# Kernel optimization log

Hardware: AMD Instinct MI355X
Metric: run time of the kernel (lower is better)

Reference implementation:

```python
import jax, jax.numpy as jnp
import numpy as np
from jax.scipy.special import logsumexp

TEMPERATURE = 0.1
EPS = 1e-8  # matches torch F.cosine_similarity eps


def setup_inputs() -> dict:
    key = jax.random.key(0)
    k1, k2 = jax.random.split(key)
    N, D, NUM_CLASSES = 8192, 256, 64
    embeddings = jax.random.normal(k1, (N, D), dtype=jnp.float32)
    target = jax.random.randint(k2, (N,), 0, NUM_CLASSES, dtype=jnp.int64)
    return {"embeddings": embeddings, "target": target}


def reference(embeddings, target):
    N = target.shape[0]
    # cosine similarity: normalize rows, then a single GEMM for all pairs
    norms = jnp.linalg.norm(embeddings, axis=-1, keepdims=True)
    e = embeddings / jnp.maximum(norms, EPS)
    sim = (e @ e.T) / TEMPERATURE  # [N, N]

    pos = target[:, None] == target[None, :]  # [N, N] bool, incl. diagonal
    diag = jnp.eye(N, dtype=bool)
    neg_inf = jnp.asarray(-jnp.inf, dtype=sim.dtype)

    # denominator: negatives only (positives masked to -inf)
    lse_neg = logsumexp(jnp.where(pos, neg_inf, sim), axis=1)
    # numerator: positives excluding self (diagonal masked to -inf)
    lse_pos = logsumexp(jnp.where(pos & ~diag, sim, neg_inf), axis=1)

    loss = lse_neg - lse_pos
    return loss.sum()
```

## Files before the change

kernel.cpp:

```cpp
#include <hip/hip_runtime.h>
#include <hip/hip_bf16.h>
#include <stdint.h>
#include <math.h>

#define NROWS 8192
#define DIM   256
#define RB    256
#define BI    128
#define JSUB  64
#define NBJS  8
#define JBLK  (JSUB*NBJS)
#define NG    (NROWS/JBLK)
#define NIT   (NROWS/BI)
#define NCLS  64
#define CAP   256

typedef __attribute__((ext_vector_type(4)))  int   int4v;
typedef __attribute__((ext_vector_type(8)))  int   int8v;
typedef __attribute__((ext_vector_type(16))) float floatx16;

typedef const __attribute__((address_space(1))) uint32_t gas_u32;
typedef __attribute__((address_space(3))) uint32_t las_u32;

#define SCALE_1_16 0x7B7B7B7B
#define L2E10      14.4269504088896f
#define CA_SCALE   (L2E10 * 16.0f)
#define CB_SCALE   16.0f

#if __has_builtin(__builtin_amdgcn_exp2f)
#define EXP2(x) __builtin_amdgcn_exp2f(x)
#else
#define EXP2(x) exp2f(x)
#endif

__device__ __forceinline__ void gload_lds16(const void* g, void* l) {
    __builtin_amdgcn_global_load_lds((gas_u32*)(uintptr_t)g,
                                     (las_u32*)(uintptr_t)l, 16, 0, 0);
}

__global__ __launch_bounds__(256) void normalize_kernel(const float* __restrict__ emb,
                                                        uint32_t* __restrict__ a8,
                                                        uint32_t* __restrict__ b8,
                                                        float* __restrict__ out)
{
    if (blockIdx.x == 0 && threadIdx.x == 0) *out = 0.f;
    int row  = blockIdx.x * 4 + (threadIdx.x >> 6);
    int lane = threadIdx.x & 63;
    float4 v = ((const float4*)(emb + (size_t)row * DIM))[lane];
    float ss = v.x*v.x + v.y*v.y + v.z*v.z + v.w*v.w;
    #pragma unroll
    for (int off = 32; off > 0; off >>= 1)
        ss += __shfl_xor(ss, off, 64);
    float inv = 1.0f / fmaxf(sqrtf(ss), 1e-8f);
    float ia = CA_SCALE * inv, ib = CB_SCALE * inv;
    int ra = __builtin_amdgcn_cvt_pk_fp8_f32(v.x * ia, v.y * ia, 0, false);
    ra     = __builtin_amdgcn_cvt_pk_fp8_f32(v.z * ia, v.w * ia, ra, true);
    int rb = __builtin_amdgcn_cvt_pk_fp8_f32(v.x * ib, v.y * ib, 0, false);
    rb     = __builtin_amdgcn_cvt_pk_fp8_f32(v.z * ib, v.w * ib, rb, true);
    a8[(size_t)row * 64 + lane] = (uint32_t)ra;
    b8[(size_t)row * 64 + lane] = (uint32_t)rb;
}

template<bool DIAG>
__device__ __forceinline__ void epi(const floatx16 acc[2],
                                    int jbs, int h, int ic0, float& ts)
{
    #pragma unroll
    for (int jt = 0; jt < 2; ++jt)
        #pragma unroll
        for (int rq = 0; rq < 4; ++rq)
            #pragma unroll
            for (int r2 = 0; r2 < 4; ++r2) {
                float v = EXP2(acc[jt][rq * 4 + r2]);
                if (DIAG) {
                    const int jg_ = jbs + jt * 32 + rq * 8 + h * 4 + r2;
                    if (jg_ == ic0) v = 0.f;
                }
                ts += v;
            }
}

__global__ __launch_bounds__(256, 4) void fused_kernel(const uint8_t* __restrict__ eA,
                                                       const uint8_t* __restrict__ eB,
                                                       const int* __restrict__ tgt,
                                                       float* __restrict__ pts,
                                                       float* __restrict__ sp)
{
    __shared__ uint8_t smem[2 * JSUB * RB];

    const int bi   = blockIdx.x;
    const int jg   = blockIdx.y;
    const int tid  = threadIdx.x;
    const int wave = tid >> 6;
    const int lane = tid & 63;
    const int col  = lane & 31;
    const int h    = lane >> 5;

    const uint8_t* pbB = eB + (size_t)(bi * BI + wave * 32 + col) * RB + h * 32;
    int8v bfr[4];
    #pragma unroll
    for (int s = 0; s < 4; ++s)
        bfr[s] = *(const int8v*)(pbB + s * 64);

    int goffA[4];
    #pragma unroll
    for (int t = 0; t < 4; ++t) {
        int s   = wave * 256 + t * 64 + lane;
        int row = s >> 4;
        int lc  = (s & 15) ^ (row & 15);
        goffA[t] = row * RB + lc * 16;
    }
    const char* gA = (const char*)(eA + (size_t)jg * JBLK * RB);

    #pragma unroll
    for (int t = 0; t < 4; ++t)
        gload_lds16(gA + goffA[t], smem + wave * 4096 + t * 1024);

    const int ic0 = bi * BI + wave * 32 + col;

    const int xm = col & 15;
    int poff[4];
    #pragma unroll
    for (int s = 0; s < 4; ++s)
        poff[s] = ((s * 4 + h * 2) ^ xm) << 4;

    __syncthreads();

    float ts = 0.f;
    const int dpair = bi - jg * 4;

    #pragma unroll
    for (int bjs = 0; bjs < NBJS; ++bjs) {
        if (bjs < NBJS - 1) {
            const char* gAn = gA + (size_t)(bjs + 1) * JSUB * RB;
            #pragma unroll
            for (int t = 0; t < 4; ++t)
                gload_lds16(gAn + goffA[t],
                            smem + ((bjs + 1) & 1) * (JSUB * RB) + wave * 4096 + t * 1024);
        }

        const uint8_t* ab = smem + (bjs & 1) * (JSUB * RB);
        floatx16 acc[2];
        #pragma unroll
        for (int jt = 0; jt < 2; ++jt)
            acc[jt] = (floatx16){0.f,0.f,0.f,0.f,0.f,0.f,0.f,0.f,
                                 0.f,0.f,0.f,0.f,0.f,0.f,0.f,0.f};

        #pragma unroll
        for (int s = 0; s < 4; ++s) {
            int8v af[2];
            #pragma unroll
            for (int jt = 0; jt < 2; ++jt) {
                const uint8_t* pa = ab + (size_t)(jt * 32 + col) * RB;
                int4v lo = *(const int4v*)(pa + poff[s]);
                int4v hi = *(const int4v*)(pa + (poff[s] ^ 16));
                af[jt] = __builtin_shufflevector(lo, hi, 0, 1, 2, 3, 4, 5, 6, 7);
            }
            #pragma unroll
            for (int jt = 0; jt < 2; ++jt)
                acc[jt] = __builtin_amdgcn_mfma_scale_f32_32x32x64_f8f6f4(
                    af[jt], bfr[s], acc[jt], 0, 0,
                    0, SCALE_1_16, 0, SCALE_1_16);
        }

        const int jbs = jg * JBLK + bjs * JSUB;
        if ((bjs >> 1) == dpair)
            epi<true >(acc, jbs, h, ic0, ts);
        else
            epi<false>(acc, jbs, h, ic0, ts);

        if (bjs < NBJS - 1)
            __syncthreads();
    }

    ts += __shfl_xor(ts, 32, 64);
    if (h == 0)
        pts[(size_t)jg * NROWS + ic0] = ts;

    if (jg != (bi >> 2)) return;
    const int c = bi;

    __syncthreads();
    int* idx = (int*)smem;
    int* cnt = (int*)(smem + CAP * 4);
    if (tid == 0) *cnt = 0;
    __syncthreads();
    int4v tv[8];
    #pragma unroll
    for (int k = 0; k < 8; ++k)
        tv[k] = *(const int4v*)(tgt + k * 1024 + tid * 4);
    #pragma unroll
    for (int k = 0; k < 8; ++k)
        #pragma unroll
        for (int r = 0; r < 4; ++r)
            if (tv[k][r] == c) {
                int p = atomicAdd(cnt, 1);
                if (p < CAP) idx[p] = k * 1024 + tid * 4 + r;
            }
    __syncthreads();
    const int M   = min(*cnt, CAP);
    const int Mp  = (M + 31) & ~31;
    const int nbt = Mp >> 5;

    for (int bt = wave; bt < nbt; bt += 4) {
        const int b = bt * 32 + col;
        const uint8_t* pb = eB + (size_t)idx[min(b, M - 1)] * RB + h * 32;
        int8v bpr[4];
        #pragma unroll
        for (int s = 0; s < 4; ++s)
            bpr[s] = *(const int8v*)(pb + s * 64);
        float psum = 0.f;
        for (int at = 0; at < nbt; ++at) {
            const uint8_t* pa = eA + (size_t)idx[min(at * 32 + col, M - 1)] * RB + h * 32;
            floatx16 acc = (floatx16){0.f,0.f,0.f,0.f,0.f,0.f,0.f,0.f,
                                      0.f,0.f,0.f,0.f,0.f,0.f,0.f,0.f};
            #pragma unroll
            for (int s = 0; s < 4; ++s) {
                int8v af = *(const int8v*)(pa + s * 64);
                acc = __builtin_amdgcn_mfma_scale_f32_32x32x64_f8f6f4(
                    af, bpr[s], acc, 0, 0, 0, SCALE_1_16, 0, SCALE_1_16);
            }
            #pragma unroll
            for (int rq = 0; rq < 4; ++rq)
                #pragma unroll
                for (int r2 = 0; r2 < 4; ++r2) {
                    const int a = at * 32 + rq * 8 + h * 4 + r2;
                    float v = EXP2(acc[rq * 4 + r2]);
                    psum += (a != b && a < M) ? v : 0.f;
                }
        }
        psum += __shfl_xor(psum, 32, 64);
        if (h == 0 && b < M) sp[idx[b]] = psum;
    }
}

__global__ __launch_bounds__(256) void finalize_kernel(const float* __restrict__ pts,
                                                       const float* __restrict__ sp,
                                                       float* __restrict__ out)
{
    const int i = blockIdx.x * 256 + threadIdx.x;
    float st = 0.f;
    #pragma unroll
    for (int t = 0; t < NG; ++t)
        st += pts[(size_t)t * NROWS + i];
    const float spv = sp[i];
    const float ns  = st - spv;
    float loss = logf(ns) - logf(spv);
    #pragma unroll
    for (int off = 32; off > 0; off >>= 1)
        loss += __shfl_xor(loss, off, 64);
    __shared__ float w4[4];
    if ((threadIdx.x & 63) == 0) w4[threadIdx.x >> 6] = loss;
    __syncthreads();
    if (threadIdx.x == 0)
        atomicAdd(out, w4[0] + w4[1] + w4[2] + w4[3]);
}

extern "C" void kernel_launch(void* const* d_in, const int* in_sizes, int n_in,
                              void* d_out, int out_size, void* d_ws, size_t ws_size,
                              hipStream_t stream)
{
    (void)in_sizes; (void)n_in; (void)out_size; (void)ws_size;
    const float* emb = (const float*)d_in[0];
    const int*   tgt = (const int*)d_in[1];
    float*       out = (float*)d_out;

    uint32_t* a8  = (uint32_t*)d_ws;
    uint32_t* b8  = a8 + (size_t)NROWS * 64;
    float*    pts = (float*)(b8 + (size_t)NROWS * 64);
    float*    sp  = pts + (size_t)NG * NROWS;

    normalize_kernel<<<NROWS / 4, 256, 0, stream>>>(emb, a8, b8, out);

    dim3 grid(NIT, NG);
    fused_kernel<<<grid, 256, 0, stream>>>(
        (const uint8_t*)a8, (const uint8_t*)b8, tgt, pts, sp);

    finalize_kernel<<<NROWS / 256, 256, 0, stream>>>(pts, sp, out);
}
```

Baseline: 97.47 us.

## Hoist class bucketing into a separate kernel and spread positive-pair tiles across blocks

Moves the per-class index bucketing out of the fused kernel into a small bucket_kernel that also zeroes the positive-sum buffer. The same-class positive-sum work, previously done serially by one block per class (one block in each of 16 groups of the grid), is now split so that each wave across the class's 16 blocks computes one 32x32 tile and accumulates into sp with atomicAdd. This removes the tail where a few blocks did extra serial MFMA loops, at the cost of an extra kernel launch and float atomics, which are nondeterministic.

After: 89.50 us. 8.2% less time.

```diff
diff --git a/kernel.cpp b/kernel.cpp
--- a/kernel.cpp
+++ b/kernel.cpp
@@ -61,6 +61,30 @@
     b8[(size_t)row * 64 + lane] = (uint32_t)rb;
 }
 
+__global__ __launch_bounds__(256) void bucket_kernel(const int* __restrict__ tgt,
+                                                     int* __restrict__ cidx,
+                                                     int* __restrict__ ccnt,
+                                                     float* __restrict__ sp)
+{
+    __shared__ int cnt;
+    const int c = blockIdx.x, tid = threadIdx.x;
+    if (tid == 0) cnt = 0;
+    if (tid < 128) sp[c * 128 + tid] = 0.f;
+    __syncthreads();
+    #pragma unroll
+    for (int k = 0; k < 8; ++k) {
+        int4v tv = *(const int4v*)(tgt + k * 1024 + tid * 4);
+        #pragma unroll
+        for (int r = 0; r < 4; ++r)
+            if (tv[r] == c) {
+                int p = atomicAdd(&cnt, 1);
+                if (p < CAP) cidx[c * CAP + p] = k * 1024 + tid * 4 + r;
+            }
+    }
+    __syncthreads();
+    if (tid == 0) ccnt[c] = min(cnt, CAP);
+}
+
 template<bool DIAG>
 __device__ __forceinline__ void epi(const floatx16 acc[2],
                                     int jbs, int h, int ic0, float& ts)
@@ -82,7 +106,8 @@
 
 __global__ __launch_bounds__(256, 4) void fused_kernel(const uint8_t* __restrict__ eA,
                                                        const uint8_t* __restrict__ eB,
-                                                       const int* __restrict__ tgt,
+                                                       const int* __restrict__ cidx,
+                                                       const int* __restrict__ ccnt,
                                                        float* __restrict__ pts,
                                                        float* __restrict__ sp)
 {
@@ -177,61 +202,46 @@
     if (h == 0)
         pts[(size_t)jg * NROWS + ic0] = ts;
 
-    if (jg != (bi >> 2)) return;
-    const int c = bi;
-
-    __syncthreads();
-    int* idx = (int*)smem;
-    int* cnt = (int*)(smem + CAP * 4);
-    if (tid == 0) *cnt = 0;
-    __syncthreads();
-    int4v tv[8];
-    #pragma unroll
-    for (int k = 0; k < 8; ++k)
-        tv[k] = *(const int4v*)(tgt + k * 1024 + tid * 4);
-    #pragma unroll
-    for (int k = 0; k < 8; ++k)
-        #pragma unroll
-        for (int r = 0; r < 4; ++r)
-            if (tv[k][r] == c) {
-                int p = atomicAdd(cnt, 1);
-                if (p < CAP) idx[p] = k * 1024 + tid * 4 + r;
-            }
-    __syncthreads();
-    const int M   = min(*cnt, CAP);
-    const int Mp  = (M + 31) & ~31;
-    const int nbt = Mp >> 5;
-
-    for (int bt = wave; bt < nbt; bt += 4) {
-        const int b = bt * 32 + col;
-        const uint8_t* pb = eB + (size_t)idx[min(b, M - 1)] * RB + h * 32;
-        int8v bpr[4];
-        #pragma unroll
-        for (int s = 0; s < 4; ++s)
-            bpr[s] = *(const int8v*)(pb + s * 64);
-        float psum = 0.f;
-        for (int at = 0; at < nbt; ++at) {
-            const uint8_t* pa = eA + (size_t)idx[min(at * 32 + col, M - 1)] * RB + h * 32;
-            floatx16 acc = (floatx16){0.f,0.f,0.f,0.f,0.f,0.f,0.f,0.f,
-                                      0.f,0.f,0.f,0.f,0.f,0.f,0.f,0.f};
-            #pragma unroll
-            for (int s = 0; s < 4; ++s) {
-                int8v af = *(const int8v*)(pa + s * 64);
-                acc = __builtin_amdgcn_mfma_scale_f32_32x32x64_f8f6f4(
-                    af, bpr[s], acc, 0, 0, 0, SCALE_1_16, 0, SCALE_1_16);
-            }
-            #pragma unroll
-            for (int rq = 0; rq < 4; ++rq)
-                #pragma unroll
-                for (int r2 = 0; r2 < 4; ++r2) {
-                    const int a = at * 32 + rq * 8 + h * 4 + r2;
-                    float v = EXP2(acc[rq * 4 + r2]);
-                    psum += (a != b && a < M) ? v : 0.f;
-                }
+    const int c   = bi;
+    const int M   = ccnt[c];
+    const int nbt = (M + 31) >> 5;
+    const int w64 = jg * 4 + wave;
+    const int bt  = w64 >> 3;
+    const int at  = w64 & 7;
+    if (bt >= nbt || at >= nbt) return;
+
+    const int* idx = cidx + c * CAP;
+    const int b    = bt * 32 + col;
+    const int bidx = idx[min(b, M - 1)];
+
+    const uint8_t* pb2 = eB + (size_t)bidx * RB + h * 32;
+    int8v bpr[4];
+    #pragma unroll
+    for (int s = 0; s < 4; ++s)
+        bpr[s] = *(const int8v*)(pb2 + s * 64);
+
+    const uint8_t* pa2 = eA + (size_t)idx[min(at * 32 + col, M - 1)] * RB + h * 32;
+    floatx16 acc2 = (floatx16){0.f,0.f,0.f,0.f,0.f,0.f,0.f,0.f,
+                               0.f,0.f,0.f,0.f,0.f,0.f,0.f,0.f};
+    #pragma unroll
+    for (int s = 0; s < 4; ++s) {
+        int8v af = *(const int8v*)(pa2 + s * 64);
+        acc2 = __builtin_amdgcn_mfma_scale_f32_32x32x64_f8f6f4(
+            af, bpr[s], acc2, 0, 0, 0, SCALE_1_16, 0, SCALE_1_16);
+    }
+
+    float psum = 0.f;
+    #pragma unroll
+    for (int rq = 0; rq < 4; ++rq)
+        #pragma unroll
+        for (int r2 = 0; r2 < 4; ++r2) {
+            const int a = at * 32 + rq * 8 + h * 4 + r2;
+            float v = EXP2(acc2[rq * 4 + r2]);
+            psum += (a != b && a < M) ? v : 0.f;
         }
-        psum += __shfl_xor(psum, 32, 64);
-        if (h == 0 && b < M) sp[idx[b]] = psum;
-    }
+    psum += __shfl_xor(psum, 32, 64);
+    if (h == 0 && b < M)
+        atomicAdd(&sp[bidx], psum);
 }
 
 __global__ __launch_bounds__(256) void finalize_kernel(const float* __restrict__ pts,
@@ -265,16 +275,20 @@
     const int*   tgt = (const int*)d_in[1];
     float*       out = (float*)d_out;
 
-    uint32_t* a8  = (uint32_t*)d_ws;
-    uint32_t* b8  = a8 + (size_t)NROWS * 64;
-    float*    pts = (float*)(b8 + (size_t)NROWS * 64);
-    float*    sp  = pts + (size_t)NG * NROWS;
+    uint32_t* a8   = (uint32_t*)d_ws;
+    uint32_t* b8   = a8 + (size_t)NROWS * 64;
+    float*    pts  = (float*)(b8 + (size_t)NROWS * 64);
+    float*    sp   = pts + (size_t)NG * NROWS;
+    int*      cidx = (int*)(sp + NROWS);
+    int*      ccnt = cidx + NCLS * CAP;
 
     normalize_kernel<<<NROWS / 4, 256, 0, stream>>>(emb, a8, b8, out);
+
+    bucket_kernel<<<NCLS, 256, 0, stream>>>(tgt, cidx, ccnt, sp);
 
     dim3 grid(NIT, NG);
     fused_kernel<<<grid, 256, 0, stream>>>(
-        (const uint8_t*)a8, (const uint8_t*)b8, tgt, pts, sp);
+        (const uint8_t*)a8, (const uint8_t*)b8, cidx, ccnt, pts, sp);
 
     finalize_kernel<<<NROWS / 256, 256, 0, stream>>>(pts, sp, out);
 }
```
